# Performance work log

Measured on AMD Instinct MI355X. Metric: run time of the kernel, lower is better.

## Reference

```python
import jax, jax.numpy as jnp
import numpy as np

N, G, CIN, COUT, K, M, H, W = 4, 8, 256, 256, 3, 4, 32, 32


def setup_inputs() -> dict:
    key = jax.random.key(0)
    ks = jax.random.split(key, 12)
    s = 0.02
    return {
        "x": jax.random.normal(ks[0], (N, G, CIN, H, W), jnp.float32),
        # grouped 1x1 conv weights: (G, out_per_group, in_per_group)
        "wq": jax.random.normal(ks[1], (G, COUT, CIN), jnp.float32) * s,
        "wk": jax.random.normal(ks[2], (G, COUT, CIN), jnp.float32) * s,
        "wv": jax.random.normal(ks[3], (G, COUT, CIN), jnp.float32) * s,
        # relative embeddings: height varies over K1, width over K2
        "hm": jax.random.normal(ks[4], (G * COUT // 2, K, 1), jnp.float32),
        "wm": jax.random.normal(ks[5], (G * COUT // 2, 1, K), jnp.float32),
        "w_conv": jax.random.normal(ks[6], (G, CIN, COUT), jnp.float32) * s,
        "b_conv": jnp.zeros((G, CIN), jnp.float32),
        "w_f1": jax.random.normal(ks[7], (G, COUT, CIN), jnp.float32) * s,
        "b_f1": jnp.zeros((G, COUT), jnp.float32),
        "w_f2": jax.random.normal(ks[8], (G, CIN, COUT), jnp.float32) * s,
        "b_f2": jnp.zeros((G, CIN), jnp.float32),
        "g1": jnp.ones((CIN // M,), jnp.float32),
        "b1": jnp.zeros((CIN // M,), jnp.float32),
        "g2": jnp.ones((CIN // M,), jnp.float32),
        "b2": jnp.zeros((CIN // M,), jnp.float32),
    }


def _gconv(x, w, b=None):
    # grouped 1x1 conv: x (N,G,Ci,H,W), w (G,Co,Ci)
    y = jnp.einsum('ngihw,goi->ngohw', x, w)
    return y if b is None else y + b[None, :, :, None, None]


def _unfold(x4, k):
    # nn.Unfold(k, 1, (k-1)//2, 1): x4 (N,C,H,W) -> patches (N,C,k,k,H,W)
    p = (k - 1) // 2
    hh, ww = x4.shape[2], x4.shape[3]
    xp = jnp.pad(x4, ((0, 0), (0, 0), (p, p), (p, p)))
    return jnp.stack(
        [jnp.stack([xp[:, :, i:i + hh, j:j + ww] for j in range(k)], axis=2)
         for i in range(k)], axis=2)


def _skip(t, m):
    # 'N G (M D) H W -> N (H W) M G D'
    n, g, c, h, w = t.shape
    d = c // m
    return t.reshape(n, g, m, d, h, w).transpose(0, 4, 5, 2, 1, 3).reshape(n, h * w, m, g, d)


def _ln(t, gamma, beta, eps=1e-5):
    mu = t.mean(-1, keepdims=True)
    var = t.var(-1, keepdims=True)  # biased, matches torch LayerNorm
    return (t - mu) / jnp.sqrt(var + eps) * gamma + beta


def _forward(x, wq, wk, wv, hm, wm, w_conv, b_conv, w_f1, b_f1, w_f2, b_f2, g1, b1, g2, b2):
    n, g, c, h, w = x.shape
    m = M
    dout = COUT // m
    q = _gconv(x, wq).reshape(n, g, m, dout, h, w)
    k0 = _gconv(x, wk).reshape(n, g * COUT, h, w)
    kp = _unfold(k0, K)  # (n, G*COUT, K, K, h, w)
    half = g * COUT // 2
    kp = jnp.concatenate(
        [kp[:, :half] + hm[None, :, :, :, None, None],
         kp[:, half:] + wm[None, :, :, :, None, None]], axis=1)
    kp = kp.reshape(n, g, m, dout, K, K, h, w)
    v0 = _gconv(x, wv).reshape(n, g * COUT, h, w)
    vp = _unfold(v0, K).reshape(n, g, m, dout, K, K, h, w)
    # per (pixel, head): q (G,D) @ k (D, G*KK) -> softmax -> @ v (G*KK, D)
    scores = jnp.einsum('ngmdhw,nemdijhw->nhwmgeij', q, kp)
    attn = jax.nn.softmax(scores.reshape(n, h, w, m, g, -1), axis=-1)
    attn = attn.reshape(n, h, w, m, g, g, K, K)
    av = jnp.einsum('nhwmgeij,nemdijhw->ngmdhw', attn, vp)
    y = av.reshape(n, g, m * dout, h, w)
    y = _gconv(y, w_conv, b_conv)  # (n, g, CIN, h, w)
    t = _ln(_skip(x, m) + _skip(y, m), g1, b1)  # (n, hw, m, g, d)
    # NB: source does .reshape (not a permute) here -> intentional layout scramble
    y = t.reshape(n, g, -1, h, w)
    f = _gconv(jax.nn.relu(_gconv(y, w_f1, b_f1)), w_f2, b_f2)
    t2 = _ln(_skip(y, m) + _skip(f, m), g2, b2)
    return t2.reshape(n, g, -1, h, w)


def reference(x, wq, wk, wv, hm, wm, w_conv, b_conv, w_f1, b_f1, w_f2, b_f2, g1, b1, g2, b2):
    return _forward(x, wq, wk, wv, hm, wm, w_conv, b_conv, w_f1, b_f1, w_f2, b_f2, g1, b1, g2, b2)
```

## Files before the change

kernel.cpp:

```cpp
#include <hip/hip_runtime.h>


typedef unsigned short u16;
typedef unsigned int u32;
typedef __attribute__((ext_vector_type(8))) short bf16x8;
typedef __attribute__((ext_vector_type(4))) float f32x4;

__device__ __forceinline__ u32 fbits(float f) { u32 x; __builtin_memcpy(&x, &f, 4); return x; }
__device__ __forceinline__ float bf2f(u32 v) {
    u32 x = v << 16; float f; __builtin_memcpy(&f, &x, 4); return f;
}
__device__ __forceinline__ u16 f2bf(float f) {
    u32 x = fbits(f);
    u32 r = x + 0x7fffu + ((x >> 16) & 1u);
    return (u16)(r >> 16);
}
__device__ __forceinline__ u32 pack2bf(float a, float b) {
    return __builtin_amdgcn_perm(fbits(b) + 0x8000u, fbits(a) + 0x8000u, 0x07060302u);
}

__device__ __forceinline__ void unpack8(uint4 u, float* o) {
    o[0] = bf2f(u.x & 0xffff); o[1] = bf2f(u.x >> 16);
    o[2] = bf2f(u.y & 0xffff); o[3] = bf2f(u.y >> 16);
    o[4] = bf2f(u.z & 0xffff); o[5] = bf2f(u.z >> 16);
    o[6] = bf2f(u.w & 0xffff); o[7] = bf2f(u.w >> 16);
}
__device__ __forceinline__ void ld8bf(const u16* p, float* o) { unpack8(*(const uint4*)p, o); }
__device__ __forceinline__ void ld8f(const float* p, float* o) {
    float4 a = *(const float4*)p, b = *(const float4*)(p + 4);
    o[0] = a.x; o[1] = a.y; o[2] = a.z; o[3] = a.w;
    o[4] = b.x; o[5] = b.y; o[6] = b.z; o[7] = b.w;
}
__device__ __forceinline__ void st4bf(u16* p, const float* v) {
    ushort4 s; s.x = f2bf(v[0]); s.y = f2bf(v[1]); s.z = f2bf(v[2]); s.w = f2bf(v[3]);
    *(ushort4*)p = s;
}

#if defined(__has_builtin)
#if __has_builtin(__builtin_amdgcn_fdot2_f32_bf16)
#define HAVE_BFDOT 1
#endif
#endif
#ifdef HAVE_BFDOT
typedef __attribute__((ext_vector_type(2))) __bf16 v2bf;
__device__ __forceinline__ float dot2bf(u32 a, u32 b, float c) {
    return __builtin_amdgcn_fdot2_f32_bf16(__builtin_bit_cast(v2bf, a),
                                           __builtin_bit_cast(v2bf, b), c, false);
}
#else
__device__ __forceinline__ float dot2bf(u32 a, u32 b, float c) {
    return c + bf2f(a & 0xffff) * bf2f(b & 0xffff) + bf2f(a >> 16) * bf2f(b >> 16);
}
#endif
__device__ __forceinline__ float dot8bf(uint4 a, uint4 b, float c) {
    c = dot2bf(a.x, b.x, c); c = dot2bf(a.y, b.y, c);
    c = dot2bf(a.z, b.z, c); c = dot2bf(a.w, b.w, c);
    return c;
}

__global__ __launch_bounds__(256) void xcast_kernel(const float* __restrict__ x,
                                                    u16* __restrict__ xb) {
    const size_t i = ((size_t)blockIdx.x * 256 + threadIdx.x) * 8;
    float4 a = *(const float4*)(x + i), b = *(const float4*)(x + i + 4);
    uint4 o;
    o.x = pack2bf(a.x, a.y); o.y = pack2bf(a.z, a.w);
    o.z = pack2bf(b.x, b.y); o.w = pack2bf(b.z, b.w);
    *(uint4*)(xb + i) = o;
}

template<int BMODE, int OUTMODE, int RELU>
__global__ __launch_bounds__(256) void gemm_kernel(
    const float* __restrict__ A0, const float* __restrict__ A1,
    const float* __restrict__ A2, const void* __restrict__ B,
    const float* __restrict__ bias,
    u16* __restrict__ O0, u16* __restrict__ O1, u16* __restrict__ O2) {
    __shared__ __align__(16) char smem[OUTMODE == 1 ? 64 * 132 * 4 : 20480];
    u16* Al = (u16*)smem;
    u16* Bl = (u16*)(smem + 10240);
    float* Cl = (float*)smem;

    const int tid = threadIdx.x;
    const int pt = blockIdx.x, ot = blockIdx.y;
    const int ngz = blockIdx.z, sel = ngz >> 5, ng = ngz & 31;
    const float* A = (sel == 0) ? A0 : (sel == 1) ? A1 : A2;
    u16* out      = (sel == 0) ? O0 : (sel == 1) ? O1 : O2;
    const int n = ng >> 3, g = ng & 7;
    const int p0 = pt << 7, o0 = ot << 7;
    const float* Ag = A + (size_t)g * 65536;

    const int l = tid & 63, w = tid >> 6;
    const int mq = w >> 1;
    const int mw = mq << 6, nw = (w & 1) << 6;
    const int lrow = l & 15, lk = (l >> 4) << 3;

    f32x4 acc[4][4];
    #pragma unroll
    for (int i = 0; i < 4; i++)
        #pragma unroll
        for (int j = 0; j < 4; j++) acc[i][j] = (f32x4){0.f, 0.f, 0.f, 0.f};

    for (int k0 = 0; k0 < 256; k0 += 32) {
        {
            const int r = tid >> 1, cb = (tid & 1) << 4;
            const float* src = Ag + (size_t)(o0 + r) * 256 + k0 + cb;
            u32* dst = (u32*)&Al[r * 40 + cb];
            #pragma unroll
            for (int q = 0; q < 4; q++) {
                float4 f = *(const float4*)(src + q * 4);
                dst[q * 2]     = pack2bf(f.x, f.y);
                dst[q * 2 + 1] = pack2bf(f.z, f.w);
            }
        }
        if (BMODE == 2) {
            const int r = tid >> 1, cb = (tid & 1) << 4;
            const u16* src = (const u16*)B + (size_t)(n * 1024 + p0 + r) * 2048 + g * 256 + k0 + cb;
            *(uint4*)&Bl[r * 40 + cb]     = *(const uint4*)src;
            *(uint4*)&Bl[r * 40 + cb + 8] = *(const uint4*)(src + 8);
        } else {
            const int kp = tid & 15, po = tid >> 4;
            const u16* src = (const u16*)B + (size_t)(ng * 256 + k0 + 2 * kp) * 1024 + p0 + po * 8;
            uint4 r0 = *(const uint4*)src;
            uint4 r1 = *(const uint4*)(src + 1024);
            u32 a0[4] = { r0.x, r0.y, r0.z, r0.w };
            u32 a1[4] = { r1.x, r1.y, r1.z, r1.w };
            #pragma unroll
            for (int j = 0; j < 4; j++) {
                u32 w0 = __builtin_amdgcn_perm(a1[j], a0[j], 0x05040100u);
                u32 w1 = __builtin_amdgcn_perm(a1[j], a0[j], 0x07060302u);
                *(u32*)&Bl[(po * 8 + 2 * j    ) * 40 + 2 * kp] = w0;
                *(u32*)&Bl[(po * 8 + 2 * j + 1) * 40 + 2 * kp] = w1;
            }
        }
        __syncthreads();
        bf16x8 af[4], bfg[4];
        #pragma unroll
        for (int i = 0; i < 4; i++) af[i]  = *(const bf16x8*)&Al[(mw + i * 16 + lrow) * 40 + lk];
        #pragma unroll
        for (int j = 0; j < 4; j++) bfg[j] = *(const bf16x8*)&Bl[(nw + j * 16 + lrow) * 40 + lk];
        #pragma unroll
        for (int i = 0; i < 4; i++)
            #pragma unroll
            for (int j = 0; j < 4; j++)
                acc[i][j] = __builtin_amdgcn_mfma_f32_16x16x32_bf16(af[i], bfg[j], acc[i][j], 0, 0, 0);
        __syncthreads();
    }

    if (OUTMODE == 0) {
        #pragma unroll
        for (int i = 0; i < 4; i++) {
            const int orow = o0 + mw + i * 16 + ((l >> 4) << 2);
            #pragma unroll
            for (int j = 0; j < 4; j++) {
                const int p = p0 + nw + j * 16 + lrow;
                float v4[4] = { acc[i][j].x, acc[i][j].y, acc[i][j].z, acc[i][j].w };
                st4bf(out + (size_t)(n * 1024 + p) * 2048 + g * 256 + orow, v4);
            }
        }
    } else {
        for (int ph = 0; ph < 2; ph++) {
            __syncthreads();
            if (mq == ph) {
                #pragma unroll
                for (int i = 0; i < 4; i++) {
                    const int rl = i * 16 + ((l >> 4) << 2);
                    #pragma unroll
                    for (int j = 0; j < 4; j++) {
                        const int c = nw + j * 16 + lrow;
                        Cl[(rl    ) * 132 + c] = acc[i][j].x;
                        Cl[(rl + 1) * 132 + c] = acc[i][j].y;
                        Cl[(rl + 2) * 132 + c] = acc[i][j].z;
                        Cl[(rl + 3) * 132 + c] = acc[i][j].w;
                    }
                }
            }
            __syncthreads();
            {
                const int row = tid >> 2, pc = (tid & 3) << 5;
                const int og = o0 + ph * 64 + row;
                const float bb = bias ? bias[g * 256 + og] : 0.f;
                u32 pk[16];
                #pragma unroll
                for (int q = 0; q < 8; q++) {
                    float4 f = *(const float4*)&Cl[row * 132 + pc + q * 4];
                    float a0 = f.x + bb, a1 = f.y + bb, a2 = f.z + bb, a3 = f.w + bb;
                    if (RELU) {
                        a0 = fmaxf(a0, 0.f); a1 = fmaxf(a1, 0.f);
                        a2 = fmaxf(a2, 0.f); a3 = fmaxf(a3, 0.f);
                    }
                    pk[q * 2]     = pack2bf(a0, a1);
                    pk[q * 2 + 1] = pack2bf(a2, a3);
                }
                u16* dst = out + (size_t)(ng * 256 + og) * 1024 + p0 + pc;
                #pragma unroll
                for (int q = 0; q < 4; q++) *(uint4*)(dst + q * 8) = *(uint4*)&pk[q * 4];
            }
        }
    }
}

__device__ __forceinline__ int swzb(int off) { return off ^ (((off >> 9) & 7) << 4); }

__global__ __launch_bounds__(256, 4) void attn_kernel(
    const u16* __restrict__ qt, const u16* __restrict__ kt,
    const u16* __restrict__ vt, const float* __restrict__ hm,
    const float* __restrict__ wm, u16* __restrict__ av) {
    __shared__ __align__(16) char kvb[9 * 4096];
    const int tid = threadIdx.x;
    const int bx = blockIdx.x, n = blockIdx.y;
    const int p = ((bx & 7) << 7) | (bx >> 3);
    const int ph = p >> 5, pw = p & 31;
    const size_t nimg = (size_t)n * 1024;

    int npix[9]; unsigned inb = 0;
    #pragma unroll
    for (int ij = 0; ij < 9; ij++) {
        int hs = ph + ij / 3 - 1, wc = pw + ij % 3 - 1;
        npix[ij] = hs * 32 + wc;
        if (((unsigned)hs < 32u) && ((unsigned)wc < 32u)) inb |= (1u << ij);
    }

    const int e_th = tid & 7, g_th = (tid >> 3) & 7, m_th = tid >> 6;

    uint4 qv[8];
    {
        const u16* qp = qt + (nimg + p) * 2048 + g_th * 256 + m_th * 64;
        #pragma unroll
        for (int c8 = 0; c8 < 8; c8++) qv[c8] = *(const uint4*)(qp + c8 * 8);
    }

    {
        const int c0 = tid << 3;
        const float* rb = (tid < 128) ? (hm + (size_t)c0 * 3)
                                      : (wm + (size_t)(c0 - 1024) * 3);
        float r[24];
        #pragma unroll
        for (int q = 0; q < 6; q++) {
            float4 f = *(const float4*)(rb + q * 4);
            r[q * 4] = f.x; r[q * 4 + 1] = f.y; r[q * 4 + 2] = f.z; r[q * 4 + 3] = f.w;
        }
        #pragma unroll
        for (int idx = 0; idx < 3; idx++) {
            u32 pk[4];
            #pragma unroll
            for (int j = 0; j < 4; j++)
                pk[j] = pack2bf(r[(2 * j) * 3 + idx], r[(2 * j + 1) * 3 + idx]);
            *(uint4*)(kvb + swzb(idx * 4096 + c0 * 2)) = *(uint4*)pk;
        }
    }
    __syncthreads();

    float qrel3[3] = {};
    {
        const int ckr = e_th * 256 + m_th * 64;
        #pragma unroll
        for (int c8 = 0; c8 < 8; c8++) {
            #pragma unroll
            for (int idx = 0; idx < 3; idx++) {
                uint4 rv = *(const uint4*)(kvb + swzb(idx * 4096 + (ckr + c8 * 8) * 2));
                qrel3[idx] = dot8bf(qv[c8], rv, qrel3[idx]);
            }
        }
    }
    __syncthreads();

    const int stoff = ((tid >> 3) & 3) * 1024 + (tid >> 5) * 128
                    + ((((tid & 7) ^ (tid >> 5)) & 7) << 4);
    const int c_s = tid << 3;
    #pragma unroll
    for (int ij = 0; ij < 9; ij++)
        if (inb & (1u << ij))
            *(uint4*)(kvb + ij * 4096 + stoff) =
                *(const uint4*)(kt + (nimg + npix[ij]) * 2048 + c_s);
    __syncthreads();

    float sc[9] = {};
    const int qkb = m_th * 1024 + e_th * 128;
    #pragma unroll
    for (int c8 = 0; c8 < 8; c8++) {
        const int sw = ((c8 ^ e_th) & 7) << 4;
        #pragma unroll
        for (int ij = 0; ij < 9; ij++)
            if (inb & (1u << ij)) {
                uint4 kv = *(const uint4*)(kvb + ij * 4096 + qkb + sw);
                sc[ij] = dot8bf(qv[c8], kv, sc[ij]);
            }
    }
    #pragma unroll
    for (int ij = 0; ij < 9; ij++)
        sc[ij] += qrel3[(e_th < 4) ? (ij / 3) : (ij % 3)];

    float mx = sc[0];
    #pragma unroll
    for (int ij = 1; ij < 9; ij++) mx = fmaxf(mx, sc[ij]);
    mx = fmaxf(mx, __shfl_xor(mx, 1));
    mx = fmaxf(mx, __shfl_xor(mx, 2));
    mx = fmaxf(mx, __shfl_xor(mx, 4));
    float sum = 0.f;
    #pragma unroll
    for (int ij = 0; ij < 9; ij++) { sc[ij] = __expf(sc[ij] - mx); sum += sc[ij]; }
    sum += __shfl_xor(sum, 1); sum += __shfl_xor(sum, 2); sum += __shfl_xor(sum, 4);
    const float rinv = 1.f / sum;
    #pragma unroll
    for (int ij = 0; ij < 9; ij++) sc[ij] *= rinv;

    __syncthreads();

    #pragma unroll
    for (int ij = 0; ij < 9; ij++)
        if (inb & (1u << ij))
            *(uint4*)(kvb + ij * 4096 + stoff) =
                *(const uint4*)(vt + (nimg + npix[ij]) * 2048 + c_s);
    __syncthreads();

    const int l = tid & 63;
    const int db = l & 7, srcb = l & 0x38;
    const int avb = m_th * 1024;
    float acc[8] = {};
    #pragma unroll
    for (int ij = 0; ij < 9; ij++) {
        if (!(inb & (1u << ij))) continue;
        #pragma unroll
        for (int e = 0; e < 8; e++) {
            const float a = __shfl(sc[ij], srcb | e);
            uint4 vv = *(const uint4*)(kvb + ij * 4096 + avb + e * 128 + (((db ^ e) & 7) << 4));
            float v8[8];
            unpack8(vv, v8);
            #pragma unroll
            for (int u = 0; u < 8; u++) acc[u] += a * v8[u];
        }
    }
    const int c0 = (l >> 3) * 256 + m_th * 64 + (db << 3);
    st4bf(av + (nimg + p) * 2048 + c0, acc);
    st4bf(av + (nimg + p) * 2048 + c0 + 4, acc + 4);
}

__global__ __launch_bounds__(256) void ln_kernel(
    const void* __restrict__ A, int aF32, const void* __restrict__ B, int bF32,
    const float* __restrict__ gamma, const float* __restrict__ beta,
    void* __restrict__ out, int outF32) {
    __shared__ float s[64][68];
    __shared__ float red[2][4][64];
    __shared__ float mu_s[64], rs_s[64], gam[64], bet[64];
    const int tid = threadIdx.x;
    const int pt = blockIdx.x, m = blockIdx.y, ng = blockIdx.z;
    const int n = ng >> 3, g = ng & 7;
    const int p0 = pt << 6;
    if (tid < 64) { gam[tid] = gamma[tid]; bet[tid] = beta[tid]; }

    const int sd = tid >> 2, sp = (tid & 3) << 4;
    {
        const size_t base = (size_t)((n * 8 + g) * 256 + m * 64 + sd) * 1024 + p0 + sp;
        #pragma unroll
        for (int half = 0; half < 2; half++) {
            float a8[8], b8[8];
            if (aF32) ld8f((const float*)A + base + half * 8, a8);
            else      ld8bf((const u16*)A + base + half * 8, a8);
            if (bF32) ld8f((const float*)B + base + half * 8, b8);
            else      ld8bf((const u16*)B + base + half * 8, b8);
            #pragma unroll
            for (int u = 0; u < 8; u++) s[sd][sp + half * 8 + u] = a8[u] + b8[u];
        }
    }
    __syncthreads();
    const int rp = tid & 63, rq = tid >> 6;
    float sm = 0.f, sq = 0.f;
    #pragma unroll
    for (int u = 0; u < 16; u++) { float v = s[rq * 16 + u][rp]; sm += v; sq += v * v; }
    red[0][rq][rp] = sm; red[1][rq][rp] = sq;
    __syncthreads();
    if (tid < 64) {
        float s2 = red[0][0][tid] + red[0][1][tid] + red[0][2][tid] + red[0][3][tid];
        float q2 = red[1][0][tid] + red[1][1][tid] + red[1][2][tid] + red[1][3][tid];
        float mu = s2 * (1.f / 64.f);
        float var = q2 * (1.f / 64.f) - mu * mu;
        mu_s[tid] = mu; rs_s[tid] = rsqrtf(var + 1e-5f);
    }
    __syncthreads();
    const int op = tid >> 2, od = (tid & 3) << 4;
    const float mu = mu_s[op], rs = rs_s[op];
    const size_t obase = (size_t)n * 2097152 + (size_t)(p0 + op) * 2048 + m * 512 + g * 64 + od;
    #pragma unroll
    for (int q4 = 0; q4 < 4; q4++) {
        float v4[4];
        #pragma unroll
        for (int u = 0; u < 4; u++) {
            int d = od + q4 * 4 + u;
            v4[u] = (s[d][op] - mu) * rs * gam[d] + bet[d];
        }
        if (outF32) {
            float4 f4; f4.x = v4[0]; f4.y = v4[1]; f4.z = v4[2]; f4.w = v4[3];
            *(float4*)((float*)out + obase + q4 * 4) = f4;
        } else {
            st4bf((u16*)out + obase + q4 * 4, v4);
        }
    }
}

extern "C" void kernel_launch(void* const* d_in, const int* in_sizes, int n_in,
                              void* d_out, int out_size, void* d_ws, size_t ws_size,
                              hipStream_t stream) {
    const float* x   = (const float*)d_in[0];
    const float* wq  = (const float*)d_in[1];
    const float* wk  = (const float*)d_in[2];
    const float* wv  = (const float*)d_in[3];
    const float* hm  = (const float*)d_in[4];
    const float* wm  = (const float*)d_in[5];
    const float* wc  = (const float*)d_in[6];
    const float* bc  = (const float*)d_in[7];
    const float* wf1 = (const float*)d_in[8];
    const float* bf1 = (const float*)d_in[9];
    const float* wf2 = (const float*)d_in[10];
    const float* bf2w = (const float*)d_in[11];
    const float* g1  = (const float*)d_in[12];
    const float* b1  = (const float*)d_in[13];
    const float* g2  = (const float*)d_in[14];
    const float* b2  = (const float*)d_in[15];
    char* ws = (char*)d_ws;
    u16* bufQ = (u16*)d_out;
    u16* xb   = bufQ + 8388608;
    u16* bufK = (u16*)(ws);
    u16* bufV = (u16*)(ws + 16777216);

    const dim3 gg(8, 2, 32), gq(8, 2, 96), gb(256);
    xcast_kernel<<<dim3(4096), gb, 0, stream>>>(x, xb);
    gemm_kernel<1, 0, 0><<<gq, gb, 0, stream>>>(wq, wk, wv, xb, nullptr, bufQ, bufK, bufV);
    attn_kernel<<<dim3(1024, 4), gb, 0, stream>>>(bufQ, bufK, bufV, hm, wm, bufQ);
    gemm_kernel<2, 1, 0><<<gg, gb, 0, stream>>>(wc, wc, wc, bufQ, bc, bufK, bufK, bufK);
    ln_kernel<<<dim3(16, 4, 32), gb, 0, stream>>>(xb, 0, bufK, 0, g1, b1, bufV, 0);
    gemm_kernel<1, 1, 1><<<gg, gb, 0, stream>>>(wf1, wf1, wf1, bufV, bf1, bufQ, bufQ, bufQ);
    gemm_kernel<1, 1, 0><<<gg, gb, 0, stream>>>(wf2, wf2, wf2, bufQ, bf2w, bufK, bufK, bufK);
    ln_kernel<<<dim3(16, 4, 32), gb, 0, stream>>>(bufV, 0, bufK, 0, g2, b2, d_out, 1);
}
```

Measured before the change: 337.0 us.

## Fuse residual-add LayerNorm into GEMM epilogues and fold input cast into QKV GEMM

Removes the separate fp32-to-bf16 cast kernel so the QKV GEMM reads and packs fp32 x directly. The two standalone LayerNorm kernels are merged into the epilogues of the w_conv and w_f2 GEMMs, which add bias and residual in shared memory and normalize over 64-channel slices. The attention kernel now issues K and V global loads into registers earlier so they overlap other work. The cost is more shared memory and registers per GEMM block and a longer serialized epilogue, and the residual for LN1 now comes from fp32 x instead of the bf16 copy.

```diff
diff --git a/kernel.cpp b/kernel.cpp
--- a/kernel.cpp
+++ b/kernel.cpp
@@ -58,26 +58,22 @@
     return c;
 }
 
-__global__ __launch_bounds__(256) void xcast_kernel(const float* __restrict__ x,
-                                                    u16* __restrict__ xb) {
-    const size_t i = ((size_t)blockIdx.x * 256 + threadIdx.x) * 8;
-    float4 a = *(const float4*)(x + i), b = *(const float4*)(x + i + 4);
-    uint4 o;
-    o.x = pack2bf(a.x, a.y); o.y = pack2bf(a.z, a.w);
-    o.z = pack2bf(b.x, b.y); o.w = pack2bf(b.z, b.w);
-    *(uint4*)(xb + i) = o;
-}
-
-template<int BMODE, int OUTMODE, int RELU>
+template<int BMODE, int OM, int RELU, int RF32>
 __global__ __launch_bounds__(256) void gemm_kernel(
     const float* __restrict__ A0, const float* __restrict__ A1,
     const float* __restrict__ A2, const void* __restrict__ B,
-    const float* __restrict__ bias,
+    const float* __restrict__ bias, const void* __restrict__ resid,
+    const float* __restrict__ gamma, const float* __restrict__ beta,
     u16* __restrict__ O0, u16* __restrict__ O1, u16* __restrict__ O2) {
-    __shared__ __align__(16) char smem[OUTMODE == 1 ? 64 * 132 * 4 : 20480];
+    __shared__ __align__(16) char smem[OM >= 2 ? 37376 : (OM == 1 ? 33792 : 20480)];
     u16* Al = (u16*)smem;
     u16* Bl = (u16*)(smem + 10240);
     float* Cl = (float*)smem;
+    float* red  = (float*)(smem + 33792);
+    float* mu_s = (float*)(smem + 35840);
+    float* rs_s = (float*)(smem + 36352);
+    float* g_s  = (float*)(smem + 36864);
+    float* b_s  = (float*)(smem + 37120);
 
     const int tid = threadIdx.x;
     const int pt = blockIdx.x, ot = blockIdx.y;
@@ -88,6 +84,8 @@
     const int p0 = pt << 7, o0 = ot << 7;
     const float* Ag = A + (size_t)g * 65536;
 
+    if (OM >= 2 && tid < 64) { g_s[tid] = gamma[tid]; b_s[tid] = beta[tid]; }
+
     const int l = tid & 63, w = tid >> 6;
     const int mq = w >> 1;
     const int mw = mq << 6, nw = (w & 1) << 6;
@@ -116,7 +114,7 @@
             const u16* src = (const u16*)B + (size_t)(n * 1024 + p0 + r) * 2048 + g * 256 + k0 + cb;
             *(uint4*)&Bl[r * 40 + cb]     = *(const uint4*)src;
             *(uint4*)&Bl[r * 40 + cb + 8] = *(const uint4*)(src + 8);
-        } else {
+        } else if (BMODE == 1) {
             const int kp = tid & 15, po = tid >> 4;
             const u16* src = (const u16*)B + (size_t)(ng * 256 + k0 + 2 * kp) * 1024 + p0 + po * 8;
             uint4 r0 = *(const uint4*)src;
@@ -130,6 +128,14 @@
                 *(u32*)&Bl[(po * 8 + 2 * j    ) * 40 + 2 * kp] = w0;
                 *(u32*)&Bl[(po * 8 + 2 * j + 1) * 40 + 2 * kp] = w1;
             }
+        } else {
+            const int kp = tid & 15, po = tid >> 4;
+            const float* src = (const float*)B + (size_t)(ng * 256 + k0 + 2 * kp) * 1024 + p0 + po * 8;
+            float r0[8], r1[8];
+            ld8f(src, r0); ld8f(src + 1024, r1);
+            #pragma unroll
+            for (int j = 0; j < 8; j++)
+                *(u32*)&Bl[(po * 8 + j) * 40 + 2 * kp] = pack2bf(r0[j], r1[j]);
         }
         __syncthreads();
         bf16x8 af[4], bfg[4];
@@ -145,7 +151,7 @@
         __syncthreads();
     }
 
-    if (OUTMODE == 0) {
+    if (OM == 0) {
         #pragma unroll
         for (int i = 0; i < 4; i++) {
             const int orow = o0 + mw + i * 16 + ((l >> 4) << 2);
@@ -156,7 +162,7 @@
                 st4bf(out + (size_t)(n * 1024 + p) * 2048 + g * 256 + orow, v4);
             }
         }
-    } else {
+    } else if (OM == 1) {
         for (int ph = 0; ph < 2; ph++) {
             __syncthreads();
             if (mq == ph) {
@@ -195,6 +201,93 @@
                 for (int q = 0; q < 4; q++) *(uint4*)(dst + q * 8) = *(uint4*)&pk[q * 4];
             }
         }
+    } else {
+        for (int ph = 0; ph < 2; ph++) {
+            const int ms = (ot << 1) | ph;
+            __syncthreads();
+            if (mq == ph) {
+                #pragma unroll
+                for (int i = 0; i < 4; i++) {
+                    const int rl = i * 16 + ((l >> 4) << 2);
+                    #pragma unroll
+                    for (int j = 0; j < 4; j++) {
+                        const int c = nw + j * 16 + lrow;
+                        Cl[(rl    ) * 132 + c] = acc[i][j].x;
+                        Cl[(rl + 1) * 132 + c] = acc[i][j].y;
+                        Cl[(rl + 2) * 132 + c] = acc[i][j].z;
+                        Cl[(rl + 3) * 132 + c] = acc[i][j].w;
+                    }
+                }
+            }
+            __syncthreads();
+            {
+                const int row = tid >> 2, pc = (tid & 3) << 5;
+                const int o = (ms << 6) + row;
+                const float bb = bias[g * 256 + o];
+                const size_t rb = (size_t)(ng * 256 + o) * 1024 + p0 + pc;
+                float* cp = &Cl[row * 132 + pc];
+                #pragma unroll
+                for (int c8 = 0; c8 < 4; c8++) {
+                    float r8[8];
+                    if (RF32) ld8f((const float*)resid + rb + c8 * 8, r8);
+                    else      ld8bf((const u16*)resid + rb + c8 * 8, r8);
+                    #pragma unroll
+                    for (int u = 0; u < 8; u++) cp[c8 * 8 + u] += bb + r8[u];
+                }
+            }
+            __syncthreads();
+            {
+                const int c = tid & 127, hh = tid >> 7;
+                float sm = 0.f, sq = 0.f;
+                #pragma unroll
+                for (int r = 0; r < 32; r++) {
+                    float v = Cl[(hh * 32 + r) * 132 + c];
+                    sm += v; sq += v * v;
+                }
+                red[hh * 128 + c] = sm; red[256 + hh * 128 + c] = sq;
+            }
+            __syncthreads();
+            if (tid < 128) {
+                float s2 = red[tid] + red[128 + tid];
+                float q2 = red[256 + tid] + red[384 + tid];
+                float mu = s2 * (1.f / 64.f);
+                float var = q2 * (1.f / 64.f) - mu * mu;
+                mu_s[tid] = mu; rs_s[tid] = rsqrtf(var + 1e-5f);
+            }
+            __syncthreads();
+            {
+                const int c = tid & 127, dh = (tid >> 7) << 5;
+                const float mu = mu_s[c], rs = rs_s[c];
+                const size_t ob = (size_t)n * 2097152 + (size_t)(p0 + c) * 2048
+                                + ms * 512 + g * 64 + dh;
+                if (OM == 3) {
+                    float* op = (float*)O0 + ob;
+                    #pragma unroll
+                    for (int q4 = 0; q4 < 8; q4++) {
+                        float4 f;
+                        f.x = (Cl[(dh + q4 * 4    ) * 132 + c] - mu) * rs * g_s[dh + q4 * 4    ] + b_s[dh + q4 * 4    ];
+                        f.y = (Cl[(dh + q4 * 4 + 1) * 132 + c] - mu) * rs * g_s[dh + q4 * 4 + 1] + b_s[dh + q4 * 4 + 1];
+                        f.z = (Cl[(dh + q4 * 4 + 2) * 132 + c] - mu) * rs * g_s[dh + q4 * 4 + 2] + b_s[dh + q4 * 4 + 2];
+                        f.w = (Cl[(dh + q4 * 4 + 3) * 132 + c] - mu) * rs * g_s[dh + q4 * 4 + 3] + b_s[dh + q4 * 4 + 3];
+                        *(float4*)(op + q4 * 4) = f;
+                    }
+                } else {
+                    u16* op = O0 + ob;
+                    #pragma unroll
+                    for (int q8 = 0; q8 < 4; q8++) {
+                        u32 pk[4];
+                        #pragma unroll
+                        for (int j = 0; j < 4; j++) {
+                            const int d = dh + q8 * 8 + j * 2;
+                            float a = (Cl[(d    ) * 132 + c] - mu) * rs * g_s[d    ] + b_s[d    ];
+                            float b = (Cl[(d + 1) * 132 + c] - mu) * rs * g_s[d + 1] + b_s[d + 1];
+                            pk[j] = pack2bf(a, b);
+                        }
+                        *(uint4*)(op + q8 * 8) = *(uint4*)pk;
+                    }
+                }
+            }
+        }
     }
 }
 
@@ -220,6 +313,15 @@
     }
 
     const int e_th = tid & 7, g_th = (tid >> 3) & 7, m_th = tid >> 6;
+    const int stoff = ((tid >> 3) & 3) * 1024 + (tid >> 5) * 128
+                    + ((((tid & 7) ^ (tid >> 5)) & 7) << 4);
+    const int c_s = tid << 3;
+
+    uint4 kreg[9];
+    #pragma unroll
+    for (int ij = 0; ij < 9; ij++)
+        if (inb & (1u << ij))
+            kreg[ij] = *(const uint4*)(kt + (nimg + npix[ij]) * 2048 + c_s);
 
     uint4 qv[8];
     {
@@ -263,14 +365,15 @@
     }
     __syncthreads();
 
-    const int stoff = ((tid >> 3) & 3) * 1024 + (tid >> 5) * 128
-                    + ((((tid & 7) ^ (tid >> 5)) & 7) << 4);
-    const int c_s = tid << 3;
     #pragma unroll
     for (int ij = 0; ij < 9; ij++)
         if (inb & (1u << ij))
-            *(uint4*)(kvb + ij * 4096 + stoff) =
-                *(const uint4*)(kt + (nimg + npix[ij]) * 2048 + c_s);
+            *(uint4*)(kvb + ij * 4096 + stoff) = kreg[ij];
+    uint4 vreg[9];
+    #pragma unroll
+    for (int ij = 0; ij < 9; ij++)
+        if (inb & (1u << ij))
+            vreg[ij] = *(const uint4*)(vt + (nimg + npix[ij]) * 2048 + c_s);
     __syncthreads();
 
     float sc[9] = {};
@@ -308,8 +411,7 @@
     #pragma unroll
     for (int ij = 0; ij < 9; ij++)
         if (inb & (1u << ij))
-            *(uint4*)(kvb + ij * 4096 + stoff) =
-                *(const uint4*)(vt + (nimg + npix[ij]) * 2048 + c_s);
+            *(uint4*)(kvb + ij * 4096 + stoff) = vreg[ij];
     __syncthreads();
 
     const int l = tid & 63;
@@ -332,68 +434,6 @@
     const int c0 = (l >> 3) * 256 + m_th * 64 + (db << 3);
     st4bf(av + (nimg + p) * 2048 + c0, acc);
     st4bf(av + (nimg + p) * 2048 + c0 + 4, acc + 4);
-}
-
-__global__ __launch_bounds__(256) void ln_kernel(
-    const void* __restrict__ A, int aF32, const void* __restrict__ B, int bF32,
-    const float* __restrict__ gamma, const float* __restrict__ beta,
-    void* __restrict__ out, int outF32) {
-    __shared__ float s[64][68];
-    __shared__ float red[2][4][64];
-    __shared__ float mu_s[64], rs_s[64], gam[64], bet[64];
-    const int tid = threadIdx.x;
-    const int pt = blockIdx.x, m = blockIdx.y, ng = blockIdx.z;
-    const int n = ng >> 3, g = ng & 7;
-    const int p0 = pt << 6;
-    if (tid < 64) { gam[tid] = gamma[tid]; bet[tid] = beta[tid]; }
-
-    const int sd = tid >> 2, sp = (tid & 3) << 4;
-    {
-        const size_t base = (size_t)((n * 8 + g) * 256 + m * 64 + sd) * 1024 + p0 + sp;
-        #pragma unroll
-        for (int half = 0; half < 2; half++) {
-            float a8[8], b8[8];
-            if (aF32) ld8f((const float*)A + base + half * 8, a8);
-            else      ld8bf((const u16*)A + base + half * 8, a8);
-            if (bF32) ld8f((const float*)B + base + half * 8, b8);
-            else      ld8bf((const u16*)B + base + half * 8, b8);
-            #pragma unroll
-            for (int u = 0; u < 8; u++) s[sd][sp + half * 8 + u] = a8[u] + b8[u];
-        }
-    }
-    __syncthreads();
-    const int rp = tid & 63, rq = tid >> 6;
-    float sm = 0.f, sq = 0.f;
-    #pragma unroll
-    for (int u = 0; u < 16; u++) { float v = s[rq * 16 + u][rp]; sm += v; sq += v * v; }
-    red[0][rq][rp] = sm; red[1][rq][rp] = sq;
-    __syncthreads();
-    if (tid < 64) {
-        float s2 = red[0][0][tid] + red[0][1][tid] + red[0][2][tid] + red[0][3][tid];
-        float q2 = red[1][0][tid] + red[1][1][tid] + red[1][2][tid] + red[1][3][tid];
-        float mu = s2 * (1.f / 64.f);
-        float var = q2 * (1.f / 64.f) - mu * mu;
-        mu_s[tid] = mu; rs_s[tid] = rsqrtf(var + 1e-5f);
-    }
-    __syncthreads();
-    const int op = tid >> 2, od = (tid & 3) << 4;
-    const float mu = mu_s[op], rs = rs_s[op];
-    const size_t obase = (size_t)n * 2097152 + (size_t)(p0 + op) * 2048 + m * 512 + g * 64 + od;
-    #pragma unroll
-    for (int q4 = 0; q4 < 4; q4++) {
-        float v4[4];
-        #pragma unroll
-        for (int u = 0; u < 4; u++) {
-            int d = od + q4 * 4 + u;
-            v4[u] = (s[d][op] - mu) * rs * gam[d] + bet[d];
-        }
-        if (outF32) {
-            float4 f4; f4.x = v4[0]; f4.y = v4[1]; f4.z = v4[2]; f4.w = v4[3];
-            *(float4*)((float*)out + obase + q4 * 4) = f4;
-        } else {
-            st4bf((u16*)out + obase + q4 * 4, v4);
-        }
-    }
 }
 
 extern "C" void kernel_launch(void* const* d_in, const int* in_sizes, int n_in,
@@ -417,17 +457,18 @@
     const float* b2  = (const float*)d_in[15];
     char* ws = (char*)d_ws;
     u16* bufQ = (u16*)d_out;
-    u16* xb   = bufQ + 8388608;
     u16* bufK = (u16*)(ws);
     u16* bufV = (u16*)(ws + 16777216);
 
     const dim3 gg(8, 2, 32), gq(8, 2, 96), gb(256);
-    xcast_kernel<<<dim3(4096), gb, 0, stream>>>(x, xb);
-    gemm_kernel<1, 0, 0><<<gq, gb, 0, stream>>>(wq, wk, wv, xb, nullptr, bufQ, bufK, bufV);
+    gemm_kernel<3, 0, 0, 0><<<gq, gb, 0, stream>>>(
+        wq, wk, wv, x, nullptr, nullptr, nullptr, nullptr, bufQ, bufK, bufV);
     attn_kernel<<<dim3(1024, 4), gb, 0, stream>>>(bufQ, bufK, bufV, hm, wm, bufQ);
-    gemm_kernel<2, 1, 0><<<gg, gb, 0, stream>>>(wc, wc, wc, bufQ, bc, bufK, bufK, bufK);
-    ln_kernel<<<dim3(16, 4, 32), gb, 0, stream>>>(xb, 0, bufK, 0, g1, b1, bufV, 0);
-    gemm_kernel<1, 1, 1><<<gg, gb, 0, stream>>>(wf1, wf1, wf1, bufV, bf1, bufQ, bufQ, bufQ);
-    gemm_kernel<1, 1, 0><<<gg, gb, 0, stream>>>(wf2, wf2, wf2, bufQ, bf2w, bufK, bufK, bufK);
-    ln_kernel<<<dim3(16, 4, 32), gb, 0, stream>>>(bufV, 0, bufK, 0, g2, b2, d_out, 1);
-}
+    gemm_kernel<2, 2, 0, 1><<<gg, gb, 0, stream>>>(
+        wc, wc, wc, bufQ, bc, x, g1, b1, bufV, bufV, bufV);
+    gemm_kernel<1, 1, 1, 0><<<gg, gb, 0, stream>>>(
+        wf1, wf1, wf1, bufV, bf1, nullptr, nullptr, nullptr, bufK, bufK, bufK);
+    gemm_kernel<1, 3, 0, 0><<<gg, gb, 0, stream>>>(
+        wf2, wf2, wf2, bufK, bf2w, bufV, g2, b2,
+        (u16*)d_out, (u16*)d_out, (u16*)d_out);
+}
```

Result: slower. 383.0 us (+13.6%).
